# Optimization experiments

Measured on AMD Instinct MI355X. Metric: run time of the kernel, lower is better.

Reference implementation:

```python
import jax, jax.numpy as jnp
import numpy as np
import math

D = 1024
FFN = 4096
NHEADS = 8
HEAD_DIM = D // NHEADS
RL_DIM = 4
LN_EPS = 1e-5


def _layer_norm(x, gamma, beta):
    mu = jnp.mean(x, axis=-1, keepdims=True)
    var = jnp.var(x, axis=-1, keepdims=True)
    return (x - mu) * jax.lax.rsqrt(var + LN_EPS) * gamma + beta


def setup_inputs() -> dict:
    key = jax.random.key(0)
    ks = jax.random.split(key, 12)
    B, L = 2, 2048
    s = 1.0 / math.sqrt(D)
    inp = {
        "h": jax.random.normal(ks[0], (B, L, D), dtype=jnp.float32),
        "rh": jax.random.normal(ks[1], (B, L, RL_DIM), dtype=jnp.float32),
        "Wq": jax.random.normal(ks[2], (D, D), dtype=jnp.float32) * s,
        "Wk": jax.random.normal(ks[3], (D, D), dtype=jnp.float32) * s,
        "Wv": jax.random.normal(ks[4], (D, D), dtype=jnp.float32) * s,
        "Wo": jax.random.normal(ks[5], (D, D), dtype=jnp.float32) * s,
        "Wrk": jax.random.normal(ks[6], (RL_DIM, RL_DIM), dtype=jnp.float32) * 0.5,
        "Wrq": jax.random.normal(ks[7], (RL_DIM, RL_DIM), dtype=jnp.float32) * 0.5,
        "W1": jax.random.normal(ks[8], (D, FFN), dtype=jnp.float32) * s,
        "b1": jnp.zeros((FFN,), dtype=jnp.float32),
        "W2": jax.random.normal(ks[9], (FFN, D), dtype=jnp.float32) / math.sqrt(FFN),
        "b2": jnp.zeros((D,), dtype=jnp.float32),
        "g1": jnp.ones((D,), dtype=jnp.float32),
        "be1": jnp.zeros((D,), dtype=jnp.float32),
        "g2": jnp.ones((D,), dtype=jnp.float32),
        "be2": jnp.zeros((D,), dtype=jnp.float32),
    }
    return inp


def reference(h, rh, Wq, Wk, Wv, Wo, Wrk, Wrq, W1, b1, W2, b2, g1, be1, g2, be2):
    B, L, _ = h.shape
    q = h @ Wq  # [B, L, D]
    k = h @ Wk
    v = h @ Wv
    # Faithful to the torch code: .view() reshapes (NOT transposes).
    q_ = q.reshape(B, NHEADS, L, HEAD_DIM)
    k_ = k.reshape(B, NHEADS, L, HEAD_DIM)
    v_ = v.reshape(B, NHEADS, L, HEAD_DIM)
    k_t = k_.reshape(B, NHEADS, HEAD_DIM, L)  # reshape, not transpose, as in source
    score = jnp.einsum("bnld,bndm->bnlm", q_, k_t) / math.sqrt(HEAD_DIM)
    # relative-position bias (rl=True path)
    r_k = rh @ Wrk  # [B, L, rl_dim]
    r_q = rh @ Wrq
    r_q_ = r_q[:, None]  # [B, 1, L, rl_dim]
    r_k_t = r_k[:, None].reshape(B, 1, RL_DIM, L)  # reshape, as in source
    score = score + jnp.einsum("bnlr,bnrm->bnlm", r_q_, r_k_t) / 2.0
    attn = jax.nn.softmax(score, axis=-1)
    context = jnp.einsum("bnlm,bnmd->bnld", attn, v_)
    h_sa = context.reshape(B, L, D) @ Wo
    h1 = _layer_norm(h_sa + h, g1, be1)
    hf = jax.nn.relu(h1 @ W1 + b1) @ W2 + b2
    h2 = _layer_norm(h1 + hf, g2, be2)
    return h2
```

## Files before the change

### kernel.cpp

```cpp
#include <hip/hip_runtime.h>

typedef __bf16 bf16;
typedef __bf16 bf16x8 __attribute__((ext_vector_type(8)));
typedef __bf16 bf16x4 __attribute__((ext_vector_type(4)));
typedef float  f32x4  __attribute__((ext_vector_type(4)));

#define D_     1024
#define FFN_   4096
#define NH_    8
#define HD_    128
#define L_     2048
#define B_     2
#define ROWS_  4096
#define PAIRS_ 16
#define KT_    64
#define PSTR   72
#define ALPHA_  0.08838834764831845f
#define RSCALE_ 5.656854249492381f

__device__ __forceinline__ void async16(const bf16* g, bf16* l) {
    __builtin_amdgcn_global_load_lds(
        (const __attribute__((address_space(1))) unsigned int*)g,
        (__attribute__((address_space(3))) unsigned int*)l, 16, 0, 0);
}
__device__ __forceinline__ f32x4 MFMA(bf16x8 a, bf16x8 b, f32x4 c) {
    return __builtin_amdgcn_mfma_f32_16x16x32_bf16(a, b, c, 0, 0, 0);
}

__global__ void cvt_bf16_kernel(const float* __restrict__ in, bf16* __restrict__ out) {
    long i = ((long)blockIdx.x * 256 + threadIdx.x) * 4;
    float4 v = *(const float4*)(in + i);
    bf16x4 o = {(bf16)v.x, (bf16)v.y, (bf16)v.z, (bf16)v.w};
    *(bf16x4*)(out + i) = o;
}

template<typename TI>
__global__ void transpose_to_bf16(const TI* __restrict__ in, bf16* __restrict__ out,
                                  int r, int c, long sIn, long sOut) {
    __shared__ bf16 t[32][33];
    long zi = (long)blockIdx.z * sIn;
    long zo = (long)blockIdx.z * sOut;
    int x0 = blockIdx.x * 32, y0 = blockIdx.y * 32;
    int tx = threadIdx.x & 31, ty = threadIdx.x >> 5;
#pragma unroll
    for (int i = 0; i < 4; i++)
        t[ty + i * 8][tx] = (bf16)in[zi + (long)(y0 + ty + i * 8) * c + x0 + tx];
    __syncthreads();
#pragma unroll
    for (int i = 0; i < 4; i++)
        out[zo + (long)(x0 + ty + i * 8) * r + y0 + tx] = t[tx][ty + i * 8];
}

__global__ void rqk_kernel(const float* __restrict__ rh, const float* __restrict__ Wrq,
                           const float* __restrict__ Wrk, float* __restrict__ rq,
                           float* __restrict__ rk) {
    int t = blockIdx.x * 256 + threadIdx.x;
    float4 r = *(const float4*)(rh + (long)t * 4);
    float q[4], k[4];
#pragma unroll
    for (int c = 0; c < 4; c++) {
        q[c] = r.x * Wrq[c] + r.y * Wrq[4 + c] + r.z * Wrq[8 + c] + r.w * Wrq[12 + c];
        k[c] = r.x * Wrk[c] + r.y * Wrk[4 + c] + r.z * Wrk[8 + c] + r.w * Wrk[12 + c];
    }
    float4 qo = {q[0], q[1], q[2], q[3]};
    float4 ko = {k[0], k[1], k[2], k[3]};
    *(float4*)(rq + (long)t * 4) = qo;
    *(float4*)(rk + (long)t * 4) = ko;
}

template<int BM, int EPI>
__launch_bounds__(256)
__global__ void gemm128(const bf16* __restrict__ A, const bf16* __restrict__ Bt,
                        void* __restrict__ Cv, const float* __restrict__ bias,
                        int M, int N, int K, int lda, int ldb,
                        long sA, long sB, long sC, float alpha) {
    constexpr int RF = (BM == 128) ? 4 : 2;
    __shared__ __align__(16) bf16 As[BM * 32];
    __shared__ __align__(16) bf16 Bs[128 * 32];
    const int tid  = threadIdx.x;
    const int wave = tid >> 6, lane = tid & 63;
    const int quad = lane >> 4, mr = lane & 15;
    const int bM = blockIdx.x * BM, bN = blockIdx.y * 128;
    A  += (long)blockIdx.z * sA;
    Bt += (long)blockIdx.z * sB;
    const int wr = (wave >> 1) * (BM / 2), wc = (wave & 1) * 64;

    f32x4 acc[RF][4];
#pragma unroll
    for (int r = 0; r < RF; r++)
#pragma unroll
        for (int c = 0; c < 4; c++) { f32x4 z = {0.f, 0.f, 0.f, 0.f}; acc[r][c] = z; }

    const int scol = (lane & 3) * 8;
    const bf16* Ag0; const bf16* Ag1 = nullptr;
    if (BM == 128) {
        const int srow = wave * 32 + (lane >> 2);
        Ag0 = A + (long)(bM + srow) * lda + scol;
        Ag1 = Ag0 + (long)16 * lda;
    } else {
        const int srow = wave * 16 + (lane >> 2);
        Ag0 = A + (long)(bM + srow) * lda + scol;
    }
    const int srowB = wave * 32 + (lane >> 2);
    const bf16* Bg0 = Bt + (long)(bN + srowB) * ldb + scol;
    const bf16* Bg1 = Bg0 + (long)16 * ldb;
    bf16* AsW = As + wave * (BM == 128 ? 1024 : 512);
    bf16* BsW = Bs + wave * 1024;

    for (int k0 = 0; k0 < K; k0 += 32) {
        if (BM == 128) { async16(Ag0, AsW); async16(Ag1, AsW + 512); Ag0 += 32; Ag1 += 32; }
        else           { async16(Ag0, AsW); Ag0 += 32; }
        async16(Bg0, BsW); async16(Bg1, BsW + 512);
        Bg0 += 32; Bg1 += 32;
        __syncthreads();
        bf16x8 af[RF], bfv[4];
#pragma unroll
        for (int r = 0; r < RF; r++)
            af[r] = *(const bf16x8*)(&As[(wr + r * 16 + mr) * 32 + quad * 8]);
#pragma unroll
        for (int c = 0; c < 4; c++)
            bfv[c] = *(const bf16x8*)(&Bs[(wc + c * 16 + mr) * 32 + quad * 8]);
#pragma unroll
        for (int r = 0; r < RF; r++)
#pragma unroll
            for (int c = 0; c < 4; c++)
                acc[r][c] = MFMA(af[r], bfv[c], acc[r][c]);
        __syncthreads();
    }

    const long zC = (long)blockIdx.z * sC;
    float bias_c[4];
    if (EPI & 1) {
#pragma unroll
        for (int c = 0; c < 4; c++) bias_c[c] = bias[bN + wc + c * 16 + mr];
    }
#pragma unroll
    for (int r = 0; r < RF; r++) {
#pragma unroll
        for (int c = 0; c < 4; c++) {
            const long col = bN + wc + c * 16 + mr;
#pragma unroll
            for (int i = 0; i < 4; i++) {
                const long row = bM + wr + r * 16 + quad * 4 + i;
                float v = acc[r][c][i] * alpha;
                if (EPI & 1) v += bias_c[c];
                if (EPI & 2) v = fmaxf(v, 0.f);
                if (EPI & 4) ((bf16*)Cv)[zC + row * (long)N + col] = (bf16)v;
                else         ((float*)Cv)[zC + row * (long)N + col] = v;
            }
        }
    }
}

template<int SPLIT>
__launch_bounds__(256, 1)
__global__ void flash_attn(const bf16* __restrict__ qb, const bf16* __restrict__ kT,
                           const bf16* __restrict__ vT, const float* __restrict__ rq,
                           const float* __restrict__ rk, bf16* __restrict__ ctx,
                           float* __restrict__ opart, float* __restrict__ osum) {
    __shared__ __align__(16) bf16  Ksh[KT_ * HD_];
    __shared__ __align__(16) bf16  Vsh[HD_ * KT_];
    __shared__ __align__(16) float rks[4 * KT_];
    __shared__ __align__(16) bf16  Ps[4][32 * PSTR];

    const int tid = threadIdx.x, wave = tid >> 6, lane = tid & 63;
    const int quad = lane >> 4, mr = lane & 15;
    const int pair = blockIdx.y, b = pair >> 3;
    const int ksp = blockIdx.z;
    const int bQ = blockIdx.x * 128;
    const long PB = (long)pair * L_ * HD_;
    const bf16* Qg = qb + PB;
    const bf16* Kg = kT + PB;
    const bf16* Vg = vT + PB;
    const float* rkb = rk + (long)b * L_ * 4;

    bf16x8 Qf[2][4], Qe[2];
#pragma unroll
    for (int f = 0; f < 2; f++) {
#pragma unroll
        for (int t = 0; t < 4; t++)
            Qf[f][t] = *(const bf16x8*)(Qg + (long)(bQ + wave * 32 + f * 16 + mr) * HD_ + t * 32 + quad * 8);
        bf16x8 z = {};
        if (quad == 0) {
            float4 v = *(const float4*)(rq + ((long)b * L_ + bQ + wave * 32 + f * 16 + mr) * 4);
            z[0] = (bf16)(v.x * RSCALE_); z[1] = (bf16)(v.y * RSCALE_);
            z[2] = (bf16)(v.z * RSCALE_); z[3] = (bf16)(v.w * RSCALE_);
        }
        Qe[f] = z;
    }

    bf16x8 ones;
#pragma unroll
    for (int j = 0; j < 8; j++) ones[j] = (bf16)1.0f;

    f32x4 O[2][8], Os[2];
#pragma unroll
    for (int f = 0; f < 2; f++) {
#pragma unroll
        for (int c = 0; c < 8; c++) { f32x4 z = {0.f, 0.f, 0.f, 0.f}; O[f][c] = z; }
        f32x4 z = {0.f, 0.f, 0.f, 0.f}; Os[f] = z;
    }

    const int tile0 = ksp * ((L_ / KT_) / SPLIT);
    const int tile1 = tile0 + (L_ / KT_) / SPLIT;
    for (int kt = tile0; kt < tile1; kt++) {
        const int kt0 = kt * KT_;
#pragma unroll
        for (int it = 0; it < 4; it++) {
            int G = it * 256 + tid;
            int r1 = G >> 4, g1 = (G & 15) ^ (r1 & 15);
            async16(Kg + (long)(kt0 + r1) * HD_ + g1 * 8, &Ksh[(it * 256 + wave * 64) * 8]);
            int r2 = G >> 3, g2 = (G & 7) ^ (r2 & 7);
            async16(Vg + (long)r2 * L_ + kt0 + g2 * 8, &Vsh[(it * 256 + wave * 64) * 8]);
        }
        if (tid < 64) {
            int r3 = tid >> 4, g3 = tid & 15;
            async16((const bf16*)(rkb + (long)r3 * L_ + kt0 + g3 * 4), (bf16*)&rks[0]);
        }
        __syncthreads();

        bf16* PsW = Ps[wave];

        f32x4 sc[4][2];
#pragma unroll
        for (int c = 0; c < 4; c++) {
            f32x4 s0 = {0.f, 0.f, 0.f, 0.f}, s1 = s0;
#pragma unroll
            for (int t = 0; t < 4; t++) {
                bf16x8 kf = *(const bf16x8*)(Ksh + (c * 16 + mr) * HD_ + (((t * 4 + quad) ^ mr) * 8));
                s0 = MFMA(Qf[0][t], kf, s0);
                s1 = MFMA(Qf[1][t], kf, s1);
            }
            bf16x8 ke = {};
            if (quad == 0) {
                ke[0] = (bf16)rks[0 * KT_ + c * 16 + mr];
                ke[1] = (bf16)rks[1 * KT_ + c * 16 + mr];
                ke[2] = (bf16)rks[2 * KT_ + c * 16 + mr];
                ke[3] = (bf16)rks[3 * KT_ + c * 16 + mr];
            }
            s0 = MFMA(Qe[0], ke, s0);
            s1 = MFMA(Qe[1], ke, s1);
            sc[c][0] = s0; sc[c][1] = s1;
        }

#pragma unroll
        for (int f = 0; f < 2; f++) {
#pragma unroll
            for (int i = 0; i < 4; i++) {
                const int prow = (f * 16 + quad * 4 + i) * PSTR;
                PsW[prow + 0 * 16 + mr] = (bf16)__expf(sc[0][f][i] * ALPHA_);
                PsW[prow + 1 * 16 + mr] = (bf16)__expf(sc[1][f][i] * ALPHA_);
                PsW[prow + 2 * 16 + mr] = (bf16)__expf(sc[2][f][i] * ALPHA_);
                PsW[prow + 3 * 16 + mr] = (bf16)__expf(sc[3][f][i] * ALPHA_);
            }
        }

#pragma unroll
        for (int t = 0; t < 2; t++) {
            bf16x8 pf0 = *(const bf16x8*)(PsW + (0 * 16 + mr) * PSTR + t * 32 + quad * 8);
            bf16x8 pf1 = *(const bf16x8*)(PsW + (1 * 16 + mr) * PSTR + t * 32 + quad * 8);
            Os[0] = MFMA(pf0, ones, Os[0]);
            Os[1] = MFMA(pf1, ones, Os[1]);
#pragma unroll
            for (int c2 = 0; c2 < 8; c2++) {
                bf16x8 vf = *(const bf16x8*)(Vsh + (c2 * 16 + mr) * KT_ + (((t * 4 + quad) ^ (mr & 7)) * 8));
                O[0][c2] = MFMA(pf0, vf, O[0][c2]);
                O[1][c2] = MFMA(pf1, vf, O[1][c2]);
            }
        }
        __syncthreads();
    }

    if (SPLIT == 1) {
        bf16* Cg = ctx + PB;
#pragma unroll
        for (int f = 0; f < 2; f++)
#pragma unroll
            for (int i = 0; i < 4; i++) {
                const float inv = 1.f / Os[f][i];
                const long row = bQ + wave * 32 + f * 16 + quad * 4 + i;
#pragma unroll
                for (int c2 = 0; c2 < 8; c2++)
                    Cg[row * HD_ + c2 * 16 + mr] = (bf16)(O[f][c2][i] * inv);
            }
    } else {
        float* Og = opart + (long)ksp * ((long)PAIRS_ * L_ * HD_) + PB;
        float* Sg = osum + (long)ksp * (PAIRS_ * L_) + pair * L_;
#pragma unroll
        for (int f = 0; f < 2; f++)
#pragma unroll
            for (int i = 0; i < 4; i++) {
                const long row = bQ + wave * 32 + f * 16 + quad * 4 + i;
#pragma unroll
                for (int c2 = 0; c2 < 8; c2++)
                    Og[row * HD_ + c2 * 16 + mr] = O[f][c2][i];
                if (mr == 0) Sg[row] = Os[f][i];
            }
    }
}

__global__ void flash_reduce(const float* __restrict__ op, const float* __restrict__ os,
                             bf16* __restrict__ ctx) {
    const long PLHD = (long)PAIRS_ * L_ * HD_;
    long e = ((long)blockIdx.x * 256 + threadIdx.x) * 4;
    long row = e >> 7;
    float4 a = *(const float4*)(op + e);
    float4 b = *(const float4*)(op + PLHD + e);
    float inv = 1.f / (os[row] + os[(long)PAIRS_ * L_ + row]);
    bf16x4 o = {(bf16)((a.x + b.x) * inv), (bf16)((a.y + b.y) * inv),
                (bf16)((a.z + b.z) * inv), (bf16)((a.w + b.w) * inv)};
    *(bf16x4*)(ctx + e) = o;
}

__global__ void layernorm_res(const float* __restrict__ x1, const float* __restrict__ x2,
                              const float* __restrict__ g, const float* __restrict__ be,
                              float* __restrict__ outf, bf16* __restrict__ outb) {
    const int row = blockIdx.x, tid = threadIdx.x;
    const long base = (long)row * D_ + tid * 4;
    float4 a = *(const float4*)(x1 + base);
    float4 b = *(const float4*)(x2 + base);
    float x[4] = {a.x + b.x, a.y + b.y, a.z + b.z, a.w + b.w};
    float s = x[0] + x[1] + x[2] + x[3];
    float s2 = x[0] * x[0] + x[1] * x[1] + x[2] * x[2] + x[3] * x[3];
#pragma unroll
    for (int off = 32; off; off >>= 1) { s += __shfl_xor(s, off, 64); s2 += __shfl_xor(s2, off, 64); }
    __shared__ float ps[4], ps2[4];
    int wave = tid >> 6, lane = tid & 63;
    if (lane == 0) { ps[wave] = s; ps2[wave] = s2; }
    __syncthreads();
    s  = ps[0] + ps[1] + ps[2] + ps[3];
    s2 = ps2[0] + ps2[1] + ps2[2] + ps2[3];
    float mean = s * (1.f / D_);
    float var  = s2 * (1.f / D_) - mean * mean;
    float rstd = rsqrtf(var + 1e-5f);
    float4 gg = *(const float4*)(g + tid * 4);
    float4 bb = *(const float4*)(be + tid * 4);
    float y0 = (x[0] - mean) * rstd * gg.x + bb.x;
    float y1 = (x[1] - mean) * rstd * gg.y + bb.y;
    float y2 = (x[2] - mean) * rstd * gg.z + bb.z;
    float y3 = (x[3] - mean) * rstd * gg.w + bb.w;
    float4 yo = {y0, y1, y2, y3};
    *(float4*)(outf + base) = yo;
    bf16x4 ob = {(bf16)y0, (bf16)y1, (bf16)y2, (bf16)y3};
    *(bf16x4*)(outb + base) = ob;
}

template<int SK>
__global__ void layernorm_res2(const float* __restrict__ parts, const float* __restrict__ b2,
                               const float* __restrict__ x2, const float* __restrict__ g,
                               const float* __restrict__ be, float* __restrict__ outf) {
    const int row = blockIdx.x, tid = threadIdx.x;
    const long base = (long)row * D_ + tid * 4;
    float4 a = *(const float4*)(parts + base);
#pragma unroll
    for (int z = 1; z < SK; z++) {
        float4 p = *(const float4*)(parts + (long)z * ROWS_ * D_ + base);
        a.x += p.x; a.y += p.y; a.z += p.z; a.w += p.w;
    }
    float4 bb2 = *(const float4*)(b2 + tid * 4);
    float4 b = *(const float4*)(x2 + base);
    float x[4] = {a.x + bb2.x + b.x, a.y + bb2.y + b.y, a.z + bb2.z + b.z, a.w + bb2.w + b.w};
    float s = x[0] + x[1] + x[2] + x[3];
    float s2 = x[0] * x[0] + x[1] * x[1] + x[2] * x[2] + x[3] * x[3];
#pragma unroll
    for (int off = 32; off; off >>= 1) { s += __shfl_xor(s, off, 64); s2 += __shfl_xor(s2, off, 64); }
    __shared__ float ps[4], ps2[4];
    int wave = tid >> 6, lane = tid & 63;
    if (lane == 0) { ps[wave] = s; ps2[wave] = s2; }
    __syncthreads();
    s  = ps[0] + ps[1] + ps[2] + ps[3];
    s2 = ps2[0] + ps2[1] + ps2[2] + ps2[3];
    float mean = s * (1.f / D_);
    float var  = s2 * (1.f / D_) - mean * mean;
    float rstd = rsqrtf(var + 1e-5f);
    float4 gg = *(const float4*)(g + tid * 4);
    float4 bb = *(const float4*)(be + tid * 4);
    float4 yo = {(x[0] - mean) * rstd * gg.x + bb.x, (x[1] - mean) * rstd * gg.y + bb.y,
                 (x[2] - mean) * rstd * gg.z + bb.z, (x[3] - mean) * rstd * gg.w + bb.w};
    *(float4*)(outf + base) = yo;
}

extern "C" void kernel_launch(void* const* d_in, const int* in_sizes, int n_in,
                              void* d_out, int out_size, void* d_ws, size_t ws_size,
                              hipStream_t stream) {
    (void)in_sizes; (void)n_in; (void)out_size;
    const float* h   = (const float*)d_in[0];
    const float* rh  = (const float*)d_in[1];
    const float* Wq  = (const float*)d_in[2];
    const float* Wk  = (const float*)d_in[3];
    const float* Wv  = (const float*)d_in[4];
    const float* Wo  = (const float*)d_in[5];
    const float* Wrk = (const float*)d_in[6];
    const float* Wrq = (const float*)d_in[7];
    const float* W1  = (const float*)d_in[8];
    const float* b1  = (const float*)d_in[9];
    const float* W2  = (const float*)d_in[10];
    const float* b2  = (const float*)d_in[11];
    const float* g1  = (const float*)d_in[12];
    const float* be1 = (const float*)d_in[13];
    const float* g2  = (const float*)d_in[14];
    const float* be2 = (const float*)d_in[15];

    char* w = (char*)d_ws;
    size_t used = 0;
    auto alloc = [&](size_t bytes) { char* p = w + used; used += (bytes + 255) & ~(size_t)255; return p; };
    bf16*  hb   = (bf16*)alloc((size_t)ROWS_ * D_ * 2);
    bf16*  Wqt  = (bf16*)alloc((size_t)D_ * D_ * 2);
    bf16*  Wkt  = (bf16*)alloc((size_t)D_ * D_ * 2);
    bf16*  Wvt  = (bf16*)alloc((size_t)D_ * D_ * 2);
    bf16*  Wot  = (bf16*)alloc((size_t)D_ * D_ * 2);
    bf16*  W1t  = (bf16*)alloc((size_t)D_ * FFN_ * 2);
    bf16*  W2t  = (bf16*)alloc((size_t)FFN_ * D_ * 2);
    bf16*  qb   = (bf16*)alloc((size_t)ROWS_ * D_ * 2);
    bf16*  kb   = (bf16*)alloc((size_t)ROWS_ * D_ * 2);
    bf16*  vb   = (bf16*)alloc((size_t)ROWS_ * D_ * 2);
    bf16*  kT   = (bf16*)alloc((size_t)ROWS_ * D_ * 2);
    bf16*  vT   = (bf16*)alloc((size_t)ROWS_ * D_ * 2);
    float* rq   = (float*)alloc((size_t)ROWS_ * 4 * 4);
    float* rk   = (float*)alloc((size_t)ROWS_ * 4 * 4);
    float* h1   = (float*)alloc((size_t)ROWS_ * D_ * 4);

    const size_t psz    = (size_t)ROWS_ * D_ * 4;
    const size_t PLHD   = (size_t)PAIRS_ * L_ * HD_;
    const size_t needKS = 2 * PLHD * 4 + 2 * (size_t)PAIRS_ * L_ * 4;
    const size_t avail  = (ws_size > used) ? ws_size - used : 0;
    const int SK = (avail >= 4 * psz) ? 4 : (avail >= 2 * psz) ? 2 : 1;
    size_t region = (size_t)SK * psz;
    const int KS = (avail >= (needKS > region ? needKS : region)) ? 2 : 1;
    if (KS == 2 && needKS > region) region = needKS;
    float* P = (float*)alloc(region);
    float* hsa   = P;
    float* Opart = P;
    float* Osum  = P + 2 * PLHD;
    bf16* ctx = hb;
    bf16* mid = qb;
    bf16* h1b = hb;

    const dim3 blk(256);
    const long BH = (long)L_ * HD_;

    cvt_bf16_kernel<<<ROWS_ * D_ / 1024, blk, 0, stream>>>(h, hb);
    transpose_to_bf16<float><<<dim3(32, 32, 1), blk, 0, stream>>>(Wq, Wqt, D_, D_, 0, 0);
    transpose_to_bf16<float><<<dim3(32, 32, 1), blk, 0, stream>>>(Wk, Wkt, D_, D_, 0, 0);
    transpose_to_bf16<float><<<dim3(32, 32, 1), blk, 0, stream>>>(Wv, Wvt, D_, D_, 0, 0);
    transpose_to_bf16<float><<<dim3(32, 32, 1), blk, 0, stream>>>(Wo, Wot, D_, D_, 0, 0);
    transpose_to_bf16<float><<<dim3(128, 32, 1), blk, 0, stream>>>(W1, W1t, D_, FFN_, 0, 0);
    transpose_to_bf16<float><<<dim3(32, 128, 1), blk, 0, stream>>>(W2, W2t, FFN_, D_, 0, 0);
    rqk_kernel<<<ROWS_ / 256, blk, 0, stream>>>(rh, Wrq, Wrk, rq, rk);
    gemm128<128, 4><<<dim3(32, 8, 3), blk, 0, stream>>>(hb, Wqt, qb, nullptr,
        ROWS_, D_, D_, D_, D_, 0, (long)D_ * D_, (long)ROWS_ * D_, 1.f);
    transpose_to_bf16<bf16><<<dim3(64, 4, PAIRS_), blk, 0, stream>>>(kb, kT, HD_, L_, BH, BH);
    transpose_to_bf16<bf16><<<dim3(4, 64, PAIRS_), blk, 0, stream>>>(vb, vT, L_, HD_, BH, BH);
    if (KS == 2) {
        flash_attn<2><<<dim3(16, 16, 2), blk, 0, stream>>>(qb, kT, vT, rq, rk, ctx, Opart, Osum);
        flash_reduce<<<PAIRS_ * L_ * HD_ / 1024, blk, 0, stream>>>(Opart, Osum, ctx);
    } else {
        flash_attn<1><<<dim3(16, 16, 1), blk, 0, stream>>>(qb, kT, vT, rq, rk, ctx, Opart, Osum);
    }
    gemm128<64, 0><<<dim3(64, 8, 1), blk, 0, stream>>>(ctx, Wot, hsa, nullptr,
        ROWS_, D_, D_, D_, D_, 0, 0, 0, 1.f);
    layernorm_res<<<ROWS_, blk, 0, stream>>>(hsa, h, g1, be1, h1, h1b);
    gemm128<128, 7><<<dim3(32, 32, 1), blk, 0, stream>>>(h1b, W1t, mid, b1,
        ROWS_, FFN_, D_, D_, D_, 0, 0, 0, 1.f);
    {
        const int KC = FFN_ / SK;
        if (SK == 4) {
            gemm128<128, 0><<<dim3(32, 8, 4), blk, 0, stream>>>(mid, W2t, P, nullptr,
                ROWS_, D_, KC, FFN_, FFN_, KC, KC, (long)ROWS_ * D_, 1.f);
            layernorm_res2<4><<<ROWS_, blk, 0, stream>>>(P, b2, h1, g2, be2, (float*)d_out);
        } else if (SK == 2) {
            gemm128<128, 0><<<dim3(32, 8, 2), blk, 0, stream>>>(mid, W2t, P, nullptr,
                ROWS_, D_, KC, FFN_, FFN_, KC, KC, (long)ROWS_ * D_, 1.f);
            layernorm_res2<2><<<ROWS_, blk, 0, stream>>>(P, b2, h1, g2, be2, (float*)d_out);
        } else {
            gemm128<128, 0><<<dim3(32, 8, 1), blk, 0, stream>>>(mid, W2t, P, nullptr,
                ROWS_, D_, FFN_, FFN_, FFN_, 0, 0, 0, 1.f);
            layernorm_res2<1><<<ROWS_, blk, 0, stream>>>(P, b2, h1, g2, be2, (float*)d_out);
        }
    }
}
```

Baseline: 422.6 us.

## Add 256x256-tile 512-thread GEMM with 4-stage async pipeline for QKV and FFN

```diff
diff --git a/kernel.cpp b/kernel.cpp
--- a/kernel.cpp
+++ b/kernel.cpp
@@ -144,6 +144,123 @@
                 const long row = bM + wr + r * 16 + quad * 4 + i;
                 float v = acc[r][c][i] * alpha;
                 if (EPI & 1) v += bias_c[c];
+                if (EPI & 2) v = fmaxf(v, 0.f);
+                if (EPI & 4) ((bf16*)Cv)[zC + row * (long)N + col] = (bf16)v;
+                else         ((float*)Cv)[zC + row * (long)N + col] = v;
+            }
+        }
+    }
+}
+
+template<int EPI>
+__launch_bounds__(512, 2)
+__global__ void gemm256(const bf16* __restrict__ A, const bf16* __restrict__ Bt,
+                        void* __restrict__ Cv, const float* __restrict__ bias,
+                        int M, int N, int K, int lda, int ldb,
+                        long sA, long sB, long sC, float alpha) {
+    __shared__ __align__(16) bf16 LA[4][256 * 32];
+    __shared__ __align__(16) bf16 LB[4][256 * 32];
+    const int tid = threadIdx.x, wave = tid >> 6, lane = tid & 63;
+    const int quad = lane >> 4, mr = lane & 15;
+    const int wr = wave >> 2, wc = wave & 3;
+    const int bM = blockIdx.x * 256, bN = blockIdx.y * 256;
+    (void)M;
+    A  += (long)blockIdx.z * sA;
+    Bt += (long)blockIdx.z * sB;
+
+    const int srow = tid >> 2;
+    const int sg   = (((tid & 3) ^ ((tid >> 3) & 3))) * 8;
+    const bf16* Ag = A  + (long)(bM + srow) * lda + sg;
+    const bf16* Bg = Bt + (long)(bN + srow) * ldb + sg;
+
+    auto stageA = [&](int slot, int kt) {
+        const bf16* s = Ag + kt * 32;
+        async16(s,                   &LA[slot][wave * 512]);
+        async16(s + (long)128 * lda, &LA[slot][4096 + wave * 512]);
+    };
+    auto stageB = [&](int slot, int kt) {
+        const bf16* s = Bg + kt * 32;
+        async16(s,                   &LB[slot][wave * 512]);
+        async16(s + (long)128 * ldb, &LB[slot][4096 + wave * 512]);
+    };
+
+    f32x4 acc[8][4];
+#pragma unroll
+    for (int f = 0; f < 8; f++)
+#pragma unroll
+        for (int n = 0; n < 4; n++) { f32x4 z = {0.f, 0.f, 0.f, 0.f}; acc[f][n] = z; }
+
+    const int gsw = (quad ^ ((mr >> 1) & 3)) * 8;
+
+    stageA(0, 0); stageB(0, 0);
+    stageA(1, 1); stageB(1, 1);
+    stageA(2, 2); stageB(2, 2);
+    asm volatile("s_waitcnt vmcnt(8)" ::: "memory");
+    __builtin_amdgcn_s_barrier();
+
+    const int NT = K >> 5;
+    for (int t = 0; t < NT; ++t) {
+        const int slot = t & 3;
+        const bf16* As = &LA[slot][0];
+        const bf16* Bs = &LB[slot][0];
+
+        bf16x8 a0[4], bb[4];
+#pragma unroll
+        for (int f = 0; f < 4; f++)
+            a0[f] = *(const bf16x8*)(As + (wr * 128 + f * 16 + mr) * 32 + gsw);
+#pragma unroll
+        for (int n = 0; n < 4; n++)
+            bb[n] = *(const bf16x8*)(Bs + (wc * 64 + n * 16 + mr) * 32 + gsw);
+        if (t + 3 < NT) stageA((t + 3) & 3, t + 3);
+        __builtin_amdgcn_s_barrier();
+        asm volatile("s_waitcnt lgkmcnt(0)" ::: "memory");
+        __builtin_amdgcn_sched_barrier(0);
+        __builtin_amdgcn_s_setprio(1);
+#pragma unroll
+        for (int f = 0; f < 4; f++)
+#pragma unroll
+            for (int n = 0; n < 4; n++)
+                acc[f][n] = MFMA(a0[f], bb[n], acc[f][n]);
+        __builtin_amdgcn_s_setprio(0);
+        __builtin_amdgcn_s_barrier();
+
+        bf16x8 a1[4];
+#pragma unroll
+        for (int f = 0; f < 4; f++)
+            a1[f] = *(const bf16x8*)(As + (wr * 128 + 64 + f * 16 + mr) * 32 + gsw);
+        if (t + 3 < NT) stageB((t + 3) & 3, t + 3);
+        __builtin_amdgcn_s_barrier();
+        asm volatile("s_waitcnt lgkmcnt(0)" ::: "memory");
+        __builtin_amdgcn_sched_barrier(0);
+        __builtin_amdgcn_s_setprio(1);
+#pragma unroll
+        for (int f = 0; f < 4; f++)
+#pragma unroll
+            for (int n = 0; n < 4; n++)
+                acc[4 + f][n] = MFMA(a1[f], bb[n], acc[4 + f][n]);
+        __builtin_amdgcn_s_setprio(0);
+        if (t < NT - 3)       asm volatile("s_waitcnt vmcnt(8)" ::: "memory");
+        else if (t == NT - 3) asm volatile("s_waitcnt vmcnt(4)" ::: "memory");
+        else if (t == NT - 2) asm volatile("s_waitcnt vmcnt(0)" ::: "memory");
+        __builtin_amdgcn_s_barrier();
+    }
+
+    const long zC = (long)blockIdx.z * sC;
+    float bias_c[4];
+    if (EPI & 1) {
+#pragma unroll
+        for (int n = 0; n < 4; n++) bias_c[n] = bias[bN + wc * 64 + n * 16 + mr];
+    }
+#pragma unroll
+    for (int f = 0; f < 8; f++) {
+#pragma unroll
+        for (int n = 0; n < 4; n++) {
+            const long col = bN + wc * 64 + n * 16 + mr;
+#pragma unroll
+            for (int i = 0; i < 4; i++) {
+                const long row = bM + wr * 128 + f * 16 + quad * 4 + i;
+                float v = acc[f][n][i] * alpha;
+                if (EPI & 1) v += bias_c[n];
                 if (EPI & 2) v = fmaxf(v, 0.f);
                 if (EPI & 4) ((bf16*)Cv)[zC + row * (long)N + col] = (bf16)v;
                 else         ((float*)Cv)[zC + row * (long)N + col] = v;
@@ -437,6 +554,7 @@
     bf16* h1b = hb;
 
     const dim3 blk(256);
+    const dim3 blk512(512);
     const long BH = (long)L_ * HD_;
 
     cvt_bf16_kernel<<<ROWS_ * D_ / 1024, blk, 0, stream>>>(h, hb);
@@ -447,7 +565,7 @@
     transpose_to_bf16<float><<<dim3(128, 32, 1), blk, 0, stream>>>(W1, W1t, D_, FFN_, 0, 0);
     transpose_to_bf16<float><<<dim3(32, 128, 1), blk, 0, stream>>>(W2, W2t, FFN_, D_, 0, 0);
     rqk_kernel<<<ROWS_ / 256, blk, 0, stream>>>(rh, Wrq, Wrk, rq, rk);
-    gemm128<128, 4><<<dim3(32, 8, 3), blk, 0, stream>>>(hb, Wqt, qb, nullptr,
+    gemm256<4><<<dim3(16, 4, 3), blk512, 0, stream>>>(hb, Wqt, qb, nullptr,
         ROWS_, D_, D_, D_, D_, 0, (long)D_ * D_, (long)ROWS_ * D_, 1.f);
     transpose_to_bf16<bf16><<<dim3(64, 4, PAIRS_), blk, 0, stream>>>(kb, kT, HD_, L_, BH, BH);
     transpose_to_bf16<bf16><<<dim3(4, 64, PAIRS_), blk, 0, stream>>>(vb, vT, L_, HD_, BH, BH);
@@ -460,16 +578,16 @@
     gemm128<64, 0><<<dim3(64, 8, 1), blk, 0, stream>>>(ctx, Wot, hsa, nullptr,
         ROWS_, D_, D_, D_, D_, 0, 0, 0, 1.f);
     layernorm_res<<<ROWS_, blk, 0, stream>>>(hsa, h, g1, be1, h1, h1b);
-    gemm128<128, 7><<<dim3(32, 32, 1), blk, 0, stream>>>(h1b, W1t, mid, b1,
+    gemm256<7><<<dim3(16, 16, 1), blk512, 0, stream>>>(h1b, W1t, mid, b1,
         ROWS_, FFN_, D_, D_, D_, 0, 0, 0, 1.f);
     {
         const int KC = FFN_ / SK;
         if (SK == 4) {
-            gemm128<128, 0><<<dim3(32, 8, 4), blk, 0, stream>>>(mid, W2t, P, nullptr,
+            gemm256<0><<<dim3(16, 4, 4), blk512, 0, stream>>>(mid, W2t, P, nullptr,
                 ROWS_, D_, KC, FFN_, FFN_, KC, KC, (long)ROWS_ * D_, 1.f);
             layernorm_res2<4><<<ROWS_, blk, 0, stream>>>(P, b2, h1, g2, be2, (float*)d_out);
         } else if (SK == 2) {
-            gemm128<128, 0><<<dim3(32, 8, 2), blk, 0, stream>>>(mid, W2t, P, nullptr,
+            gemm256<0><<<dim3(16, 4, 2), blk512, 0, stream>>>(mid, W2t, P, nullptr,
                 ROWS_, D_, KC, FFN_, FFN_, KC, KC, (long)ROWS_ * D_, 1.f);
             layernorm_res2<2><<<ROWS_, blk, 0, stream>>>(P, b2, h1, g2, be2, (float*)d_out);
         } else {
```

After: 382.4 us. -9.5%, faster.
